# Performance work log

Measured on AMD Instinct MI355X. Metric: run time of the kernel, lower is better.

Reference implementation:

```python
import jax, jax.numpy as jnp
import numpy as np

D_MODEL = 1024
NUM_HEADS = 16
D_HEAD = D_MODEL // NUM_HEADS
THETA = 10000.0


def setup_inputs() -> dict:
    key = jax.random.key(0)
    ks = jax.random.split(key, 5)
    B, S = 2, 2048
    std = np.sqrt(2.0 / (D_MODEL + D_MODEL))
    return {
        "x": jax.random.normal(ks[0], (B, S, D_MODEL), dtype=jnp.float32),
        "token_positions": jnp.arange(S, dtype=jnp.int32),
        "wq": jax.random.normal(ks[1], (D_MODEL, D_MODEL), dtype=jnp.float32) * std,
        "wk": jax.random.normal(ks[2], (D_MODEL, D_MODEL), dtype=jnp.float32) * std,
        "wv": jax.random.normal(ks[3], (D_MODEL, D_MODEL), dtype=jnp.float32) * std,
        "wo": jax.random.normal(ks[4], (D_MODEL, D_MODEL), dtype=jnp.float32) * std,
    }


def _rope(x, token_positions):
    # x: [B, H, S, D_HEAD]; token_positions: [S]
    freq_idx = jnp.arange(0, D_HEAD, 2, dtype=jnp.float32)
    inv_freq = THETA ** (-freq_idx / D_HEAD)                      # [D_HEAD/2]
    angles = token_positions.astype(jnp.float32)[:, None] * inv_freq  # [S, D_HEAD/2]
    cos = jnp.cos(angles)[None, None, :, :]
    sin = jnp.sin(angles)[None, None, :, :]
    x_even = x[..., 0::2]
    x_odd = x[..., 1::2]
    rot_even = x_even * cos - x_odd * sin
    rot_odd = x_even * sin + x_odd * cos
    # interleave pairs back: [..., pairs, 2] -> [..., D_HEAD]
    return jnp.stack((rot_even, rot_odd), axis=-1).reshape(x.shape)


def reference(x, token_positions, wq, wk, wv, wo):
    B, S, _ = x.shape
    def proj(w):
        y = jnp.einsum('bsi,oi->bso', x, w)
        return y.reshape(B, S, NUM_HEADS, D_HEAD).transpose(0, 2, 1, 3)  # [B,H,S,Dh]
    q = _rope(proj(wq), token_positions)
    k = _rope(proj(wk), token_positions)
    v = proj(wv)
    scores = jnp.einsum('bhqd,bhkd->bhqk', q, k) / jnp.sqrt(jnp.float32(D_HEAD))
    causal = jnp.tril(jnp.ones((S, S), dtype=bool))
    scores = jnp.where(causal, scores, -jnp.inf)
    probs = jax.nn.softmax(scores, axis=-1)
    attn = jnp.einsum('bhqk,bhkd->bhqd', probs, v)
    attn = attn.transpose(0, 2, 1, 3).reshape(B, S, D_MODEL)
    return jnp.einsum('bsi,oi->bso', attn, wo)
```

## Files before the change

### kernel.cpp

```cpp
#include <hip/hip_runtime.h>
#include <math.h>

#define D_MODEL 1024
#define NUM_HEADS 16
#define D_HEAD 64
#define SEQ 2048
#define BATCH 2

typedef __attribute__((ext_vector_type(8))) short short8;
typedef __attribute__((ext_vector_type(4))) short short4v;
typedef __attribute__((ext_vector_type(4))) float float4v;

__device__ __forceinline__ short f2bf(float f) {
    unsigned u = __float_as_uint(f);
    u += 0x7FFFu + ((u >> 16) & 1u);
    return (short)(u >> 16);
}

__global__ __launch_bounds__(256) void cvt_bf16_kernel(
    const float* __restrict__ x,  const float* __restrict__ wq,
    const float* __restrict__ wk, const float* __restrict__ wv,
    const float* __restrict__ wo, const int* __restrict__ pos,
    short* __restrict__ xb,  short* __restrict__ wqb,
    short* __restrict__ wkb, short* __restrict__ wvb,
    short* __restrict__ wob,
    float* __restrict__ costab, float* __restrict__ sintab)
{
    const int a = blockIdx.y;
    if (a == 5) {
        const int idx = blockIdx.x * 256 + threadIdx.x;
        if (idx < SEQ * 32) {
            const int s = idx >> 5, fi = idx & 31;
            const float p = (float)pos[s];
            const float inv_freq = exp2f((float)fi * -0.4152410118609203f);
            float sn, cs;
            sincosf(p * inv_freq, &sn, &cs);
            costab[idx] = cs;
            sintab[idx] = sn;
        }
        return;
    }
    const float* src = (a == 0) ? x : (a == 1) ? wq : (a == 2) ? wk : (a == 3) ? wv : wo;
    short* dst = (a == 0) ? xb : (a == 1) ? wqb : (a == 2) ? wkb : (a == 3) ? wvb : wob;
    const int n = (a == 0) ? (BATCH * SEQ * D_MODEL) : (D_MODEL * D_MODEL);
    const int i = (blockIdx.x * 256 + threadIdx.x) * 8;
    if (i >= n) return;
    const float4 v0 = *(const float4*)(src + i);
    const float4 v1 = *(const float4*)(src + i + 4);
    short8 r;
    r[0] = f2bf(v0.x); r[1] = f2bf(v0.y); r[2] = f2bf(v0.z); r[3] = f2bf(v0.w);
    r[4] = f2bf(v1.x); r[5] = f2bf(v1.y); r[6] = f2bf(v1.z); r[7] = f2bf(v1.w);
    *(short8*)(dst + i) = r;
}

__device__ __forceinline__ void gemm_core_db(
    const short* __restrict__ a, const short* __restrict__ b,
    short* smem, int m0, int n0, float4v acc[4][4])
{
    const int tid = threadIdx.x;
    const int lane = tid & 63;
    const int l15 = lane & 15, quad = lane >> 4;
    const int wave = tid >> 6;
    const int mw = (wave & 1) * 64, nw = (wave >> 1) * 64;
    const int srow = tid >> 2;
    const int scol = (tid & 3) * 8;
    const int ssw = (((tid & 3) ^ ((srow >> 1) & 3))) * 8;
    const int xsw = (l15 >> 1) & 3;

    const short* ag = a + (size_t)(m0 + srow) * D_MODEL + scol;
    const short* bg = b + (size_t)(n0 + srow) * D_MODEL + scol;

    short* bufA[2] = { smem,        smem + 8192 };
    short* bufB[2] = { smem + 4096, smem + 12288 };

    short8 ga0 = *(const short8*)(ag);
    short8 ga1 = *(const short8*)(ag + (size_t)64 * D_MODEL);
    short8 gb0 = *(const short8*)(bg);
    short8 gb1 = *(const short8*)(bg + (size_t)64 * D_MODEL);
    *(short8*)&bufA[0][srow * 32 + ssw]        = ga0;
    *(short8*)&bufA[0][(64 + srow) * 32 + ssw] = ga1;
    *(short8*)&bufB[0][srow * 32 + ssw]        = gb0;
    *(short8*)&bufB[0][(64 + srow) * 32 + ssw] = gb1;
    ga0 = *(const short8*)(ag + 32);
    ga1 = *(const short8*)(ag + 32 + (size_t)64 * D_MODEL);
    gb0 = *(const short8*)(bg + 32);
    gb1 = *(const short8*)(bg + 32 + (size_t)64 * D_MODEL);

    for (int k = 0; k < 32; k++) {
        __syncthreads();
        if (k + 1 < 32) {
            short* bA = bufA[(k + 1) & 1];
            short* bB = bufB[(k + 1) & 1];
            *(short8*)&bA[srow * 32 + ssw]        = ga0;
            *(short8*)&bA[(64 + srow) * 32 + ssw] = ga1;
            *(short8*)&bB[srow * 32 + ssw]        = gb0;
            *(short8*)&bB[(64 + srow) * 32 + ssw] = gb1;
        }
        if (k + 2 < 32) {
            const int off = (k + 2) * 32;
            ga0 = *(const short8*)(ag + off);
            ga1 = *(const short8*)(ag + off + (size_t)64 * D_MODEL);
            gb0 = *(const short8*)(bg + off);
            gb1 = *(const short8*)(bg + off + (size_t)64 * D_MODEL);
        }
        const short* lA = bufA[k & 1];
        const short* lB = bufB[k & 1];
        short8 af[4], bf[4];
        #pragma unroll
        for (int i = 0; i < 4; i++)
            af[i] = *(const short8*)&lA[(mw + i * 16 + l15) * 32 + (quad ^ xsw) * 8];
        #pragma unroll
        for (int i = 0; i < 4; i++)
            bf[i] = *(const short8*)&lB[(nw + i * 16 + l15) * 32 + (quad ^ xsw) * 8];
        #pragma unroll
        for (int mi = 0; mi < 4; mi++)
            #pragma unroll
            for (int ni = 0; ni < 4; ni++)
                acc[mi][ni] = __builtin_amdgcn_mfma_f32_16x16x32_bf16(
                    af[mi], bf[ni], acc[mi][ni], 0, 0, 0);
    }
}

__global__ __launch_bounds__(256) void qkv_mfma_kernel(
    const short* __restrict__ xb, const short* __restrict__ wqb,
    const short* __restrict__ wkb, const short* __restrict__ wvb,
    const float* __restrict__ costab, const float* __restrict__ sintab,
    short* __restrict__ Qb, short* __restrict__ Kb, short* __restrict__ Vt)
{
    __shared__ __align__(16) short smem[128 * 136];

    const int z = blockIdx.x >> 8;
    const int bid = blockIdx.x & 255;
    const int m0 = (bid & 31) * 128;
    const int n0 = (bid >> 5) * 128;
    const short* w = (z == 0) ? wqb : (z == 1) ? wkb : wvb;

    float4v acc[4][4];
    #pragma unroll
    for (int i = 0; i < 4; i++)
        #pragma unroll
        for (int j = 0; j < 4; j++)
            acc[i][j] = (float4v){0.f, 0.f, 0.f, 0.f};

    gemm_core_db(xb, w, smem, m0, n0, acc);

    const int tid = threadIdx.x;
    const int lane = tid & 63;
    const int l15 = lane & 15, quad = lane >> 4;
    const int wave = tid >> 6;
    const int mw = (wave & 1) * 64, nw = (wave >> 1) * 64;
    const int s_base = m0 & (SEQ - 1);
    const int bb = m0 >> 11;

    __syncthreads();

    if (z == 2) {
        #pragma unroll
        for (int ni = 0; ni < 4; ni++) {
            #pragma unroll
            for (int mi = 0; mi < 4; mi++) {
                #pragma unroll
                for (int r = 0; r < 4; r++)
                    smem[(nw + ni * 16 + l15) * 136 + mw + mi * 16 + quad * 4 + r] =
                        f2bf(acc[mi][ni][r]);
            }
        }
        __syncthreads();
        #pragma unroll
        for (int it = 0; it < 8; it++) {
            const int nloc = it * 16 + (tid >> 4);
            const int mloc = (tid & 15) * 8;
            const short8 val = *(const short8*)&smem[nloc * 136 + mloc];
            const int n = n0 + nloc;
            const int h = n >> 6, d = n & 63;
            *(short8*)(Vt + ((size_t)(bb * NUM_HEADS + h) * D_HEAD + d) * SEQ +
                       s_base + mloc) = val;
        }
    } else {
        short* dst = (z == 0) ? Qb : Kb;
        const float qs = (z == 0) ? 0.125f : 1.0f;
        #pragma unroll
        for (int ni = 0; ni < 4; ni++) {
            const int n = n0 + nw + ni * 16 + l15;
            const int d = n & 63;
            const int fi = d >> 1;
            #pragma unroll
            for (int mi = 0; mi < 4; mi++) {
                #pragma unroll
                for (int r = 0; r < 4; r++) {
                    const int mloc = mw + mi * 16 + quad * 4 + r;
                    const int ti = ((s_base + mloc) << 5) + fi;
                    const float cs = costab[ti];
                    const float sn = sintab[ti];
                    const float val = acc[mi][ni][r];
                    const float partner = __shfl_xor(val, 1, 64);
                    const float res = (l15 & 1) ? fmaf(partner, sn, val * cs)
                                                : fmaf(val, cs, -partner * sn);
                    smem[mloc * 136 + nw + ni * 16 + l15] = f2bf(res * qs);
                }
            }
        }
        __syncthreads();
        #pragma unroll
        for (int it = 0; it < 8; it++) {
            const int ri = it * 32 + (tid >> 3);
            const int mloc = ri & 127;
            const int hh = ri >> 7;
            const int nloc = hh * 64 + (tid & 7) * 8;
            const short8 val = *(const short8*)&smem[mloc * 136 + nloc];
            const int n = n0 + nloc;
            const int h = n >> 6, d = n & 63;
            *(short8*)(dst + ((size_t)(bb * NUM_HEADS + h) * SEQ + s_base + mloc) *
                       D_HEAD + d) = val;
        }
    }
}

__global__ __launch_bounds__(256) void attn_mfma_kernel(
    const short* __restrict__ Qb, const short* __restrict__ Kb,
    const short* __restrict__ Vt, short* __restrict__ Ab)
{
    __shared__ __align__(16) short lK[64 * 72];
    __shared__ __align__(16) short lV[64 * 72];
    __shared__ __align__(16) short lP[4][16 * 72];

    const int tid = threadIdx.x;
    const int lane = tid & 63;
    const int wave = tid >> 6;
    const int l15 = lane & 15;
    const int quad = lane >> 4;

    const int bh = blockIdx.x & (BATCH * NUM_HEADS - 1);
    const int qt = (SEQ / 64 - 1) - (blockIdx.x >> 5);
    const int q0w = qt * 64 + wave * 16;
    const int qcmp = q0w + l15;

    const short* Kg = Kb + (size_t)bh * SEQ * D_HEAD;
    const short* Vg = Vt + (size_t)bh * D_HEAD * SEQ;

    const short* Qrow = Qb + ((size_t)bh * SEQ + q0w + l15) * D_HEAD;
    const short8 qf0 = *(const short8*)(Qrow + quad * 8);
    const short8 qf1 = *(const short8*)(Qrow + 32 + quad * 8);

    float4v o0 = {0.f, 0.f, 0.f, 0.f}, o1 = o0, o2 = o0, o3 = o0;
    float lp = 0.f;

    const int nt = qt + 1;
    const int srow = tid >> 2;
    const int sch = (tid & 3) * 8;

    short8 k0 = *(const short8*)(Kg + (size_t)srow * D_HEAD + sch);
    short8 k1 = *(const short8*)(Kg + (size_t)srow * D_HEAD + sch + 32);
    short8 v0 = *(const short8*)(Vg + (size_t)srow * SEQ + sch);
    short8 v1 = *(const short8*)(Vg + (size_t)srow * SEQ + sch + 32);

    for (int t = 0; t < nt; t++) {
        const int kt0 = t * 64;
        __syncthreads();
        *(short8*)&lK[srow * 72 + sch]      = k0;
        *(short8*)&lK[srow * 72 + sch + 32] = k1;
        *(short8*)&lV[srow * 72 + sch]      = v0;
        *(short8*)&lV[srow * 72 + sch + 32] = v1;
        __syncthreads();
        if (t + 1 < nt) {
            k0 = *(const short8*)(Kg + (size_t)(kt0 + 64 + srow) * D_HEAD + sch);
            k1 = *(const short8*)(Kg + (size_t)(kt0 + 64 + srow) * D_HEAD + sch + 32);
            v0 = *(const short8*)(Vg + (size_t)srow * SEQ + kt0 + 64 + sch);
            v1 = *(const short8*)(Vg + (size_t)srow * SEQ + kt0 + 64 + sch + 32);
        }

        short* Pw = lP[wave];
        #pragma unroll
        for (int g = 0; g < 4; g++) {
            float4v s = {0.f, 0.f, 0.f, 0.f};
            const short8 ka = *(const short8*)&lK[(g * 16 + l15) * 72 + quad * 8];
            s = __builtin_amdgcn_mfma_f32_16x16x32_bf16(ka, qf0, s, 0, 0, 0);
            const short8 kb = *(const short8*)&lK[(g * 16 + l15) * 72 + 32 + quad * 8];
            s = __builtin_amdgcn_mfma_f32_16x16x32_bf16(kb, qf1, s, 0, 0, 0);

            const int kbase = kt0 + g * 16 + quad * 4;
            short4v pk;
            #pragma unroll
            for (int r = 0; r < 4; r++) {
                const float e = (kbase + r <= qcmp) ? __expf(s[r]) : 0.f;
                lp += e;
                pk[r] = f2bf(e);
            }
            *(short4v*)&Pw[l15 * 72 + g * 16 + quad * 4] = pk;
        }

        const short8 pa0 = *(const short8*)&lP[wave][l15 * 72 + quad * 8];
        const short8 pa1 = *(const short8*)&lP[wave][l15 * 72 + 32 + quad * 8];

        {
            const short8 va = *(const short8*)&lV[(0 * 16 + l15) * 72 + quad * 8];
            const short8 vb = *(const short8*)&lV[(0 * 16 + l15) * 72 + 32 + quad * 8];
            o0 = __builtin_amdgcn_mfma_f32_16x16x32_bf16(pa0, va, o0, 0, 0, 0);
            o0 = __builtin_amdgcn_mfma_f32_16x16x32_bf16(pa1, vb, o0, 0, 0, 0);
        }
        {
            const short8 va = *(const short8*)&lV[(1 * 16 + l15) * 72 + quad * 8];
            const short8 vb = *(const short8*)&lV[(1 * 16 + l15) * 72 + 32 + quad * 8];
            o1 = __builtin_amdgcn_mfma_f32_16x16x32_bf16(pa0, va, o1, 0, 0, 0);
            o1 = __builtin_amdgcn_mfma_f32_16x16x32_bf16(pa1, vb, o1, 0, 0, 0);
        }
        {
            const short8 va = *(const short8*)&lV[(2 * 16 + l15) * 72 + quad * 8];
            const short8 vb = *(const short8*)&lV[(2 * 16 + l15) * 72 + 32 + quad * 8];
            o2 = __builtin_amdgcn_mfma_f32_16x16x32_bf16(pa0, va, o2, 0, 0, 0);
            o2 = __builtin_amdgcn_mfma_f32_16x16x32_bf16(pa1, vb, o2, 0, 0, 0);
        }
        {
            const short8 va = *(const short8*)&lV[(3 * 16 + l15) * 72 + quad * 8];
            const short8 vb = *(const short8*)&lV[(3 * 16 + l15) * 72 + 32 + quad * 8];
            o3 = __builtin_amdgcn_mfma_f32_16x16x32_bf16(pa0, va, o3, 0, 0, 0);
            o3 = __builtin_amdgcn_mfma_f32_16x16x32_bf16(pa1, vb, o3, 0, 0, 0);
        }
    }

    lp += __shfl_xor(lp, 16, 64);
    lp += __shfl_xor(lp, 32, 64);

    const int b = bh >> 4, h = bh & 15;
    short* Ap = Ab + ((size_t)(b * SEQ) + q0w + quad * 4) * D_MODEL + h * D_HEAD;
    #pragma unroll
    for (int r = 0; r < 4; r++) {
        const float inv = 1.0f / __shfl(lp, quad * 4 + r, 64);
        Ap[(size_t)r * D_MODEL + l15]      = f2bf(o0[r] * inv);
        Ap[(size_t)r * D_MODEL + 16 + l15] = f2bf(o1[r] * inv);
        Ap[(size_t)r * D_MODEL + 32 + l15] = f2bf(o2[r] * inv);
        Ap[(size_t)r * D_MODEL + 48 + l15] = f2bf(o3[r] * inv);
    }
}

__global__ __launch_bounds__(256) void out_mfma_kernel(
    const short* __restrict__ Ab, const short* __restrict__ wob,
    float* __restrict__ out)
{
    __shared__ __align__(16) short smem[2 * 8192];

    const int bid = blockIdx.x;
    const int m0 = (bid & 31) * 128;
    const int n0 = (bid >> 5) * 128;

    float4v acc[4][4];
    #pragma unroll
    for (int i = 0; i < 4; i++)
        #pragma unroll
        for (int j = 0; j < 4; j++)
            acc[i][j] = (float4v){0.f, 0.f, 0.f, 0.f};

    gemm_core_db(Ab, wob, smem, m0, n0, acc);

    const int tid = threadIdx.x;
    const int lane = tid & 63;
    const int l15 = lane & 15, quad = lane >> 4;
    const int wave = tid >> 6;
    const int mw = (wave & 1) * 64, nw = (wave >> 1) * 64;

    #pragma unroll
    for (int mi = 0; mi < 4; mi++) {
        #pragma unroll
        for (int r = 0; r < 4; r++) {
            const int m = m0 + mw + mi * 16 + quad * 4 + r;
            float* op = out + (size_t)m * D_MODEL + n0 + nw + l15;
            #pragma unroll
            for (int ni = 0; ni < 4; ni++)
                op[ni * 16] = acc[mi][ni][r];
        }
    }
}

extern "C" void kernel_launch(void* const* d_in, const int* in_sizes, int n_in,
                              void* d_out, int out_size, void* d_ws, size_t ws_size,
                              hipStream_t stream)
{
    const float* x  = (const float*)d_in[0];
    const int*  pos = (const int*)d_in[1];
    const float* wq = (const float*)d_in[2];
    const float* wk = (const float*)d_in[3];
    const float* wv = (const float*)d_in[4];
    const float* wo = (const float*)d_in[5];
    float* out = (float*)d_out;

    const size_t nx = (size_t)BATCH * SEQ * D_MODEL;
    const size_t nw = (size_t)D_MODEL * D_MODEL;
    short* xb  = (short*)d_ws;
    short* wqb = xb + nx;
    short* wkb = wqb + nw;
    short* wvb = wkb + nw;
    short* wob = wvb + nw;
    short* Qb  = wob + nw;
    short* Kb  = Qb + nx;
    short* Vt  = Kb + nx;
    short* Ab  = Vt + nx;
    float* costab = (float*)(Ab + nx);
    float* sintab = costab + SEQ * 32;

    dim3 blk(256);
    cvt_bf16_kernel<<<dim3(2048, 6), blk, 0, stream>>>(x, wq, wk, wv, wo, pos,
                                                       xb, wqb, wkb, wvb, wob,
                                                       costab, sintab);
    qkv_mfma_kernel<<<dim3(768), blk, 0, stream>>>(xb, wqb, wkb, wvb,
                                                   costab, sintab, Qb, Kb, Vt);
    attn_mfma_kernel<<<dim3(BATCH * NUM_HEADS * (SEQ / 64)), blk, 0, stream>>>(Qb, Kb, Vt, Ab);
    out_mfma_kernel<<<dim3(256), blk, 0, stream>>>(Ab, wob, out);
}
```

Baseline: 186.7 us.

## Process 128 query rows per attention block with exp2 softmax and mask skipping

The attention kernel now handles 128 queries per block, with each wave owning two 16-row query groups that share every staged K/V tile, which halves the K/V loads per query and the block count. The 1/sqrt(d) scale now also folds in log2(e) in the Q projection, so the softmax uses the hardware exp2 instead of expf. Masking is applied only on diagonal tiles, tiles entirely above the diagonal for a wave are skipped, and packed bf16 conversion instructions replace the manual rounding. The K/V shared-memory layout is permuted to match the new fragment reads. In exchange there is more register pressure and coarser tail work per block, while the softmax still skips max subtraction as before.

```diff
diff --git a/kernel.cpp b/kernel.cpp
--- a/kernel.cpp
+++ b/kernel.cpp
@@ -10,11 +10,16 @@
 typedef __attribute__((ext_vector_type(8))) short short8;
 typedef __attribute__((ext_vector_type(4))) short short4v;
 typedef __attribute__((ext_vector_type(4))) float float4v;
+typedef __attribute__((ext_vector_type(2))) unsigned int uint2v;
 
 __device__ __forceinline__ short f2bf(float f) {
     unsigned u = __float_as_uint(f);
     u += 0x7FFFu + ((u >> 16) & 1u);
     return (short)(u >> 16);
+}
+
+__device__ __forceinline__ float fexp2(float x) {
+    return __builtin_amdgcn_exp2f(x);
 }
 
 __global__ __launch_bounds__(256) void cvt_bf16_kernel(
@@ -178,7 +183,7 @@
         }
     } else {
         short* dst = (z == 0) ? Qb : Kb;
-        const float qs = (z == 0) ? 0.125f : 1.0f;
+        const float qs = (z == 0) ? 0.18033688011112042f : 1.0f;
         #pragma unroll
         for (int ni = 0; ni < 4; ni++) {
             const int n = n0 + nw + ni * 16 + l15;
@@ -222,7 +227,7 @@
 {
     __shared__ __align__(16) short lK[64 * 72];
     __shared__ __align__(16) short lV[64 * 72];
-    __shared__ __align__(16) short lP[4][16 * 72];
+    __shared__ __align__(16) short lP[4][2][16 * 72];
 
     const int tid = threadIdx.x;
     const int lane = tid & 63;
@@ -231,23 +236,34 @@
     const int quad = lane >> 4;
 
     const int bh = blockIdx.x & (BATCH * NUM_HEADS - 1);
-    const int qt = (SEQ / 64 - 1) - (blockIdx.x >> 5);
-    const int q0w = qt * 64 + wave * 16;
-    const int qcmp = q0w + l15;
+    const int qt = (SEQ / 128 - 1) - (blockIdx.x >> 5);
+    const int q0wA = qt * 128 + wave * 32;
+    const int qcmpA = q0wA + l15;
+    const int qcmpB = q0wA + 16 + l15;
 
     const short* Kg = Kb + (size_t)bh * SEQ * D_HEAD;
     const short* Vg = Vt + (size_t)bh * D_HEAD * SEQ;
 
-    const short* Qrow = Qb + ((size_t)bh * SEQ + q0w + l15) * D_HEAD;
-    const short8 qf0 = *(const short8*)(Qrow + quad * 8);
-    const short8 qf1 = *(const short8*)(Qrow + 32 + quad * 8);
-
-    float4v o0 = {0.f, 0.f, 0.f, 0.f}, o1 = o0, o2 = o0, o3 = o0;
-    float lp = 0.f;
-
-    const int nt = qt + 1;
+    const short* QrowA = Qb + ((size_t)bh * SEQ + q0wA + l15) * D_HEAD;
+    const short8 qfA0 = *(const short8*)(QrowA + quad * 8);
+    const short8 qfA1 = *(const short8*)(QrowA + 32 + quad * 8);
+    const short* QrowB = QrowA + (size_t)16 * D_HEAD;
+    const short8 qfB0 = *(const short8*)(QrowB + quad * 8);
+    const short8 qfB1 = *(const short8*)(QrowB + 32 + quad * 8);
+
+    float4v oA[4], oB[4];
+    #pragma unroll
+    for (int j = 0; j < 4; j++) {
+        oA[j] = (float4v){0.f, 0.f, 0.f, 0.f};
+        oB[j] = (float4v){0.f, 0.f, 0.f, 0.f};
+    }
+    float lpA0 = 0.f, lpA1 = 0.f, lpB0 = 0.f, lpB1 = 0.f;
+
+    const int nt = 2 * qt + 2;
     const int srow = tid >> 2;
-    const int sch = (tid & 3) * 8;
+    const int c4  = tid & 3;
+    const int sch = c4 * 8;
+    const int w1off = srow * 72 + c4 * 16;
 
     short8 k0 = *(const short8*)(Kg + (size_t)srow * D_HEAD + sch);
     short8 k1 = *(const short8*)(Kg + (size_t)srow * D_HEAD + sch + 32);
@@ -257,10 +273,10 @@
     for (int t = 0; t < nt; t++) {
         const int kt0 = t * 64;
         __syncthreads();
-        *(short8*)&lK[srow * 72 + sch]      = k0;
-        *(short8*)&lK[srow * 72 + sch + 32] = k1;
-        *(short8*)&lV[srow * 72 + sch]      = v0;
-        *(short8*)&lV[srow * 72 + sch + 32] = v1;
+        *(short8*)&lK[w1off]     = k0;
+        *(short8*)&lK[w1off + 8] = k1;
+        *(short8*)&lV[w1off]     = v0;
+        *(short8*)&lV[w1off + 8] = v1;
         __syncthreads();
         if (t + 1 < nt) {
             k0 = *(const short8*)(Kg + (size_t)(kt0 + 64 + srow) * D_HEAD + sch);
@@ -269,67 +285,84 @@
             v1 = *(const short8*)(Vg + (size_t)srow * SEQ + kt0 + 64 + sch + 32);
         }
 
-        short* Pw = lP[wave];
-        #pragma unroll
-        for (int g = 0; g < 4; g++) {
-            float4v s = {0.f, 0.f, 0.f, 0.f};
-            const short8 ka = *(const short8*)&lK[(g * 16 + l15) * 72 + quad * 8];
-            s = __builtin_amdgcn_mfma_f32_16x16x32_bf16(ka, qf0, s, 0, 0, 0);
-            const short8 kb = *(const short8*)&lK[(g * 16 + l15) * 72 + 32 + quad * 8];
-            s = __builtin_amdgcn_mfma_f32_16x16x32_bf16(kb, qf1, s, 0, 0, 0);
-
-            const int kbase = kt0 + g * 16 + quad * 4;
-            short4v pk;
-            #pragma unroll
-            for (int r = 0; r < 4; r++) {
-                const float e = (kbase + r <= qcmp) ? __expf(s[r]) : 0.f;
-                lp += e;
-                pk[r] = f2bf(e);
+        if (kt0 <= q0wA + 31) {
+            const bool masked = (kt0 + 63 > q0wA);
+            short* PwA = &lP[wave][0][0];
+            short* PwB = &lP[wave][1][0];
+            #pragma unroll
+            for (int g = 0; g < 4; g++) {
+                float4v sA = {0.f, 0.f, 0.f, 0.f};
+                float4v sB = {0.f, 0.f, 0.f, 0.f};
+                const short8 ka = *(const short8*)&lK[(g * 16 + l15) * 72 + quad * 16];
+                const short8 kb = *(const short8*)&lK[(g * 16 + l15) * 72 + quad * 16 + 8];
+                sA = __builtin_amdgcn_mfma_f32_16x16x32_bf16(ka, qfA0, sA, 0, 0, 0);
+                sA = __builtin_amdgcn_mfma_f32_16x16x32_bf16(kb, qfA1, sA, 0, 0, 0);
+                sB = __builtin_amdgcn_mfma_f32_16x16x32_bf16(ka, qfB0, sB, 0, 0, 0);
+                sB = __builtin_amdgcn_mfma_f32_16x16x32_bf16(kb, qfB1, sB, 0, 0, 0);
+                float eA0, eA1, eA2, eA3, eB0, eB1, eB2, eB3;
+                if (masked) {
+                    const int kbase = kt0 + g * 16 + quad * 4;
+                    eA0 = (kbase + 0 <= qcmpA) ? fexp2(sA[0]) : 0.f;
+                    eA1 = (kbase + 1 <= qcmpA) ? fexp2(sA[1]) : 0.f;
+                    eA2 = (kbase + 2 <= qcmpA) ? fexp2(sA[2]) : 0.f;
+                    eA3 = (kbase + 3 <= qcmpA) ? fexp2(sA[3]) : 0.f;
+                    eB0 = (kbase + 0 <= qcmpB) ? fexp2(sB[0]) : 0.f;
+                    eB1 = (kbase + 1 <= qcmpB) ? fexp2(sB[1]) : 0.f;
+                    eB2 = (kbase + 2 <= qcmpB) ? fexp2(sB[2]) : 0.f;
+                    eB3 = (kbase + 3 <= qcmpB) ? fexp2(sB[3]) : 0.f;
+                } else {
+                    eA0 = fexp2(sA[0]); eA1 = fexp2(sA[1]);
+                    eA2 = fexp2(sA[2]); eA3 = fexp2(sA[3]);
+                    eB0 = fexp2(sB[0]); eB1 = fexp2(sB[1]);
+                    eB2 = fexp2(sB[2]); eB3 = fexp2(sB[3]);
+                }
+                lpA0 += eA0 + eA2; lpA1 += eA1 + eA3;
+                lpB0 += eB0 + eB2; lpB1 += eB1 + eB3;
+                unsigned int pa0, pa1, pb0, pb1;
+                asm("v_cvt_pk_bf16_f32 %0, %1, %2" : "=v"(pa0) : "v"(eA0), "v"(eA1));
+                asm("v_cvt_pk_bf16_f32 %0, %1, %2" : "=v"(pa1) : "v"(eA2), "v"(eA3));
+                asm("v_cvt_pk_bf16_f32 %0, %1, %2" : "=v"(pb0) : "v"(eB0), "v"(eB1));
+                asm("v_cvt_pk_bf16_f32 %0, %1, %2" : "=v"(pb1) : "v"(eB2), "v"(eB3));
+                uint2v pkA; pkA[0] = pa0; pkA[1] = pa1;
+                uint2v pkB; pkB[0] = pb0; pkB[1] = pb1;
+                *(uint2v*)&PwA[l15 * 72 + g * 16 + quad * 4] = pkA;
+                *(uint2v*)&PwB[l15 * 72 + g * 16 + quad * 4] = pkB;
             }
-            *(short4v*)&Pw[l15 * 72 + g * 16 + quad * 4] = pk;
-        }
-
-        const short8 pa0 = *(const short8*)&lP[wave][l15 * 72 + quad * 8];
-        const short8 pa1 = *(const short8*)&lP[wave][l15 * 72 + 32 + quad * 8];
-
-        {
-            const short8 va = *(const short8*)&lV[(0 * 16 + l15) * 72 + quad * 8];
-            const short8 vb = *(const short8*)&lV[(0 * 16 + l15) * 72 + 32 + quad * 8];
-            o0 = __builtin_amdgcn_mfma_f32_16x16x32_bf16(pa0, va, o0, 0, 0, 0);
-            o0 = __builtin_amdgcn_mfma_f32_16x16x32_bf16(pa1, vb, o0, 0, 0, 0);
-        }
-        {
-            const short8 va = *(const short8*)&lV[(1 * 16 + l15) * 72 + quad * 8];
-            const short8 vb = *(const short8*)&lV[(1 * 16 + l15) * 72 + 32 + quad * 8];
-            o1 = __builtin_amdgcn_mfma_f32_16x16x32_bf16(pa0, va, o1, 0, 0, 0);
-            o1 = __builtin_amdgcn_mfma_f32_16x16x32_bf16(pa1, vb, o1, 0, 0, 0);
-        }
-        {
-            const short8 va = *(const short8*)&lV[(2 * 16 + l15) * 72 + quad * 8];
-            const short8 vb = *(const short8*)&lV[(2 * 16 + l15) * 72 + 32 + quad * 8];
-            o2 = __builtin_amdgcn_mfma_f32_16x16x32_bf16(pa0, va, o2, 0, 0, 0);
-            o2 = __builtin_amdgcn_mfma_f32_16x16x32_bf16(pa1, vb, o2, 0, 0, 0);
-        }
-        {
-            const short8 va = *(const short8*)&lV[(3 * 16 + l15) * 72 + quad * 8];
-            const short8 vb = *(const short8*)&lV[(3 * 16 + l15) * 72 + 32 + quad * 8];
-            o3 = __builtin_amdgcn_mfma_f32_16x16x32_bf16(pa0, va, o3, 0, 0, 0);
-            o3 = __builtin_amdgcn_mfma_f32_16x16x32_bf16(pa1, vb, o3, 0, 0, 0);
-        }
-    }
-
-    lp += __shfl_xor(lp, 16, 64);
-    lp += __shfl_xor(lp, 32, 64);
+            const short8 paA0 = *(const short8*)&lP[wave][0][l15 * 72 + quad * 8];
+            const short8 paA1 = *(const short8*)&lP[wave][0][l15 * 72 + 32 + quad * 8];
+            const short8 paB0 = *(const short8*)&lP[wave][1][l15 * 72 + quad * 8];
+            const short8 paB1 = *(const short8*)&lP[wave][1][l15 * 72 + 32 + quad * 8];
+            #pragma unroll
+            for (int j = 0; j < 4; j++) {
+                const short8 va = *(const short8*)&lV[(j * 16 + l15) * 72 + quad * 16];
+                const short8 vb = *(const short8*)&lV[(j * 16 + l15) * 72 + quad * 16 + 8];
+                oA[j] = __builtin_amdgcn_mfma_f32_16x16x32_bf16(paA0, va, oA[j], 0, 0, 0);
+                oA[j] = __builtin_amdgcn_mfma_f32_16x16x32_bf16(paA1, vb, oA[j], 0, 0, 0);
+                oB[j] = __builtin_amdgcn_mfma_f32_16x16x32_bf16(paB0, va, oB[j], 0, 0, 0);
+                oB[j] = __builtin_amdgcn_mfma_f32_16x16x32_bf16(paB1, vb, oB[j], 0, 0, 0);
+            }
+        }
+    }
+
+    float lpA = lpA0 + lpA1;
+    lpA += __shfl_xor(lpA, 16, 64);
+    lpA += __shfl_xor(lpA, 32, 64);
+    float lpB = lpB0 + lpB1;
+    lpB += __shfl_xor(lpB, 16, 64);
+    lpB += __shfl_xor(lpB, 32, 64);
 
     const int b = bh >> 4, h = bh & 15;
-    short* Ap = Ab + ((size_t)(b * SEQ) + q0w + quad * 4) * D_MODEL + h * D_HEAD;
+    short* ApA = Ab + ((size_t)(b * SEQ) + q0wA + quad * 4) * D_MODEL + h * D_HEAD;
+    short* ApB = ApA + (size_t)16 * D_MODEL;
     #pragma unroll
     for (int r = 0; r < 4; r++) {
-        const float inv = 1.0f / __shfl(lp, quad * 4 + r, 64);
-        Ap[(size_t)r * D_MODEL + l15]      = f2bf(o0[r] * inv);
-        Ap[(size_t)r * D_MODEL + 16 + l15] = f2bf(o1[r] * inv);
-        Ap[(size_t)r * D_MODEL + 32 + l15] = f2bf(o2[r] * inv);
-        Ap[(size_t)r * D_MODEL + 48 + l15] = f2bf(o3[r] * inv);
+        const float invA = 1.0f / __shfl(lpA, quad * 4 + r, 64);
+        const float invB = 1.0f / __shfl(lpB, quad * 4 + r, 64);
+        #pragma unroll
+        for (int j = 0; j < 4; j++) {
+            ApA[(size_t)r * D_MODEL + j * 16 + l15] = f2bf(oA[j][r] * invA);
+            ApB[(size_t)r * D_MODEL + j * 16 + l15] = f2bf(oB[j][r] * invB);
+        }
     }
 }
 
@@ -403,6 +436,6 @@
                                                        costab, sintab);
     qkv_mfma_kernel<<<dim3(768), blk, 0, stream>>>(xb, wqb, wkb, wvb,
                                                    costab, sintab, Qb, Kb, Vt);
-    attn_mfma_kernel<<<dim3(BATCH * NUM_HEADS * (SEQ / 64)), blk, 0, stream>>>(Qb, Kb, Vt, Ab);
+    attn_mfma_kernel<<<dim3(BATCH * NUM_HEADS * (SEQ / 128)), blk, 0, stream>>>(Qb, Kb, Vt, Ab);
     out_mfma_kernel<<<dim3(256), blk, 0, stream>>>(Ab, wob, out);
 }
```

After: 191.1 us. 1.02x slower.
